# Performance work log

Measured on AMD Instinct MI355X. Metric: run time of the kernel, lower is better.

The kernel has to match this reference:

```python
import jax, jax.numpy as jnp
import numpy as np

N_NODES = 50000
N_EDGES = 100000
N_PAIRS = 1600000
IN_DIM = 2816
MAP_HID = 512
IN_CH = 512
HID_CH = 256
OUT_CH = 128


def _dense(x, W, b):
    return x @ W + b


def setup_inputs() -> dict:
    key = jax.random.key(0)
    ks = jax.random.split(key, 20)
    m_emb = jax.random.normal(ks[0], (N_NODES, IN_DIM), dtype=jnp.float32)
    he_v_idx_pos = jax.random.randint(ks[1], (N_PAIRS,), 0, N_NODES)
    he_e_idx_pos = jnp.sort(jax.random.randint(ks[2], (N_PAIRS,), 0, N_EDGES))
    he_v_idx_neg = jax.random.randint(ks[3], (N_PAIRS,), 0, N_NODES)
    he_e_idx_neg = jnp.sort(jax.random.randint(ks[4], (N_PAIRS,), 0, N_EDGES))

    def lin(k, din, dout):
        k1, k2 = jax.random.split(k)
        s = 1.0 / np.sqrt(din)
        W = jax.random.uniform(k1, (din, dout), minval=-s, maxval=s, dtype=jnp.float32)
        b = jax.random.uniform(k2, (dout,), minval=-s, maxval=s, dtype=jnp.float32)
        return W, b

    W0, b0 = lin(ks[5], IN_DIM, MAP_HID)
    W1, b1 = lin(ks[6], MAP_HID, MAP_HID)
    W2, b2 = lin(ks[7], MAP_HID, IN_CH)
    Wt1, bt1 = lin(ks[8], IN_CH, HID_CH)   # HGNN layer 1 theta
    Wt2, bt2 = lin(ks[9], HID_CH, OUT_CH)  # HGNN layer 2 theta

    return dict(
        m_emb=m_emb,
        he_v_idx_pos=he_v_idx_pos, he_e_idx_pos=he_e_idx_pos,
        he_v_idx_neg=he_v_idx_neg, he_e_idx_neg=he_e_idx_neg,
        W0=W0, b0=b0, W1=W1, b1=b1, W2=W2, b2=b2,
        Wt1=Wt1, bt1=bt1, Wt2=Wt2, bt2=bt2,
    )


def _hg_mean_aggr(X, v_idx, e_idx, n_edges, n_nodes):
    # v2e: mean of member-vertex features per hyperedge
    e_sum = jax.ops.segment_sum(X[v_idx], e_idx, num_segments=n_edges)
    e_cnt = jax.ops.segment_sum(jnp.ones((v_idx.shape[0],), X.dtype), e_idx, num_segments=n_edges)
    Y = e_sum / jnp.maximum(e_cnt, 1.0)[:, None]
    # e2v: mean of incident-hyperedge features per vertex
    v_sum = jax.ops.segment_sum(Y[e_idx], v_idx, num_segments=n_nodes)
    v_cnt = jax.ops.segment_sum(jnp.ones((e_idx.shape[0],), X.dtype), v_idx, num_segments=n_nodes)
    Xo = v_sum / jnp.maximum(v_cnt, 1.0)[:, None]
    return Xo, Y


def _hgnn_layer(X, v_idx, e_idx, W, b, is_last):
    X = _dense(X, W, b)
    Xo, Y = _hg_mean_aggr(X, v_idx, e_idx, N_EDGES, N_NODES)
    if not is_last:
        Xo = jax.nn.relu(Xo)  # dropout = identity in eval
    return Xo, Y


def reference(m_emb, he_v_idx_pos, he_e_idx_pos, he_v_idx_neg, he_e_idx_neg,
              W0, b0, W1, b1, W2, b2, Wt1, bt1, Wt2, bt2):
    h = jax.nn.relu(_dense(m_emb, W0, b0))
    h = jax.nn.relu(_dense(h, W1, b1))
    feat = _dense(h, W2, b2)  # [N, IN_CH]
    # num_dgnn = 0 -> skip directional conv loop
    X1, X2 = feat, feat
    X1, Y_pos = _hgnn_layer(X1, he_v_idx_pos, he_e_idx_pos, Wt1, bt1, False)
    X2, Y_neg = _hgnn_layer(X2, he_v_idx_neg, he_e_idx_neg, Wt1, bt1, False)
    X1, Y_pos = _hgnn_layer(X1, he_v_idx_pos, he_e_idx_pos, Wt2, bt2, True)
    X2, Y_neg = _hgnn_layer(X2, he_v_idx_neg, he_e_idx_neg, Wt2, bt2, True)
    return (X1, X2, Y_pos, Y_neg)
```

## Files before the change

kernel.cpp:

```cpp
#include <hip/hip_runtime.h>

#define NP 1600000
#define NNODES 50000
#define NEDGES 100000

typedef short bf16x8 __attribute__((ext_vector_type(8)));
typedef short short4b __attribute__((ext_vector_type(4)));
typedef float f32x4 __attribute__((ext_vector_type(4)));
typedef unsigned short ushort_t;

static __device__ __forceinline__ ushort_t f2bf_rne(float f) {
    __bf16 b = (__bf16)f;
    return __builtin_bit_cast(ushort_t, b);
}
static __device__ __forceinline__ float bf2f(ushort_t h) {
    union { float f; unsigned int u; } v; v.u = ((unsigned int)h) << 16;
    return v.f;
}
static __device__ __forceinline__ void addbf8(float* a, uint4 u) {
    unsigned int uu[4] = {u.x, u.y, u.z, u.w};
#pragma unroll
    for (int q = 0; q < 4; ++q) {
        union { float f; unsigned int v; } lo, hi;
        lo.v = uu[q] << 16; hi.v = uu[q] & 0xffff0000u;
        a[2 * q]     += lo.f;
        a[2 * q + 1] += hi.f;
    }
}

static __device__ __forceinline__ void gload_lds16(const void* g, void* lds) {
    __builtin_amdgcn_global_load_lds(
        (const __attribute__((address_space(1))) unsigned int*)g,
        (__attribute__((address_space(3))) unsigned int*)lds, 16, 0, 0);
}

template<bool AF32, bool DORELU, int EPI>
__global__ __launch_bounds__(256, 3) void gemm_bf1(
    const float* __restrict__ Af, const ushort_t* __restrict__ Ab,
    const ushort_t* __restrict__ Bth,
    const float* __restrict__ bias,
    float* __restrict__ Cf, ushort_t* __restrict__ Cb,
    int M, int N, int K)
{
    __shared__ ushort_t As [4][129][8];
    __shared__ ushort_t BsH[4][129][8];

    const int tid = threadIdx.x;
    const int wid = tid >> 6;
    const int lane = tid & 63;

    const int nwg = gridDim.x * gridDim.y;
    const int wg  = blockIdx.y * gridDim.x + blockIdx.x;
    const int q = nwg >> 3, r = nwg & 7;
    const int xcd = wg & 7, loc = wg >> 3;
    const int swz = (xcd < r) ? (xcd * (q + 1) + loc)
                              : (r * (q + 1) + (xcd - r) * q + loc);
    const int bn0 = (int)(swz % gridDim.x) * 128;
    const int bm0 = (int)(swz / gridDim.x) * 128;

    const int wrow0 = (wid >> 1) * 64;
    const int wcol0 = (wid & 1) * 64;
    const int kgl = lane >> 4;
    const int r16 = lane & 15;

    f32x4 acc[4][4];
#pragma unroll
    for (int i = 0; i < 4; ++i)
#pragma unroll
        for (int j = 0; j < 4; ++j) acc[i][j] = (f32x4)0.f;

    const int nk = K >> 5;

    const int a_kq   = tid & 7;
    const int a_row0 = tid >> 3;
    const float* aBase[4];
    float4 aPre[4];
    if constexpr (AF32) {
#pragma unroll
        for (int cch = 0; cch < 4; ++cch) {
            int row = cch * 32 + a_row0;
            int rr = bm0 + row; if (rr > M - 1) rr = M - 1;
            aBase[cch] = Af + (size_t)rr * K + a_kq * 4;
            aPre[cch] = *(const float4*)(aBase[cch]);
        }
    }

    for (int kt = 0; kt < nk; ++kt) {
        __syncthreads();
#pragma unroll
        for (int h = 0; h < 2; ++h) {
            int cc = bn0 + h * 64 + lane;
            gload_lds16(Bth + (size_t)cc * K + kt * 32 + wid * 8,
                        &BsH[wid][h * 64][0]);
        }
        if constexpr (AF32) {
#pragma unroll
            for (int cch = 0; cch < 4; ++cch) {
                int row = cch * 32 + a_row0;
                float4 v = aPre[cch];
                short4b hi;
                hi[0] = (short)f2bf_rne(v.x); hi[1] = (short)f2bf_rne(v.y);
                hi[2] = (short)f2bf_rne(v.z); hi[3] = (short)f2bf_rne(v.w);
                int kg = a_kq >> 1, j0 = (a_kq & 1) * 4;
                *(short4b*)&As[kg][row][j0] = hi;
            }
        } else {
#pragma unroll
            for (int h = 0; h < 2; ++h) {
                int rr = bm0 + h * 64 + lane; if (rr > M - 1) rr = M - 1;
                gload_lds16(Ab + (size_t)rr * K + kt * 32 + wid * 8,
                            &As[wid][h * 64][0]);
            }
        }
        __syncthreads();

        if constexpr (AF32) {
            if (kt + 1 < nk) {
#pragma unroll
                for (int cch = 0; cch < 4; ++cch)
                    aPre[cch] = *(const float4*)(aBase[cch] + (kt + 1) * 32);
            }
        }

        bf16x8 ah[4], bh[4];
#pragma unroll
        for (int mi = 0; mi < 4; ++mi)
            ah[mi] = *(const bf16x8*)&As[kgl][wrow0 + mi * 16 + r16][0];
#pragma unroll
        for (int ni = 0; ni < 4; ++ni)
            bh[ni] = *(const bf16x8*)&BsH[kgl][wcol0 + ni * 16 + r16][0];
#pragma unroll
        for (int mi = 0; mi < 4; ++mi)
#pragma unroll
            for (int ni = 0; ni < 4; ++ni)
                acc[mi][ni] = __builtin_amdgcn_mfma_f32_16x16x32_bf16(ah[mi], bh[ni], acc[mi][ni], 0, 0, 0);
    }

    const int rg4 = (lane >> 4) * 4;
#pragma unroll
    for (int ni = 0; ni < 4; ++ni) {
        int gcol = bn0 + wcol0 + ni * 16 + r16;
        float bb = bias[gcol];
#pragma unroll
        for (int mi = 0; mi < 4; ++mi)
#pragma unroll
            for (int rg = 0; rg < 4; ++rg) {
                int grow = bm0 + wrow0 + mi * 16 + rg4 + rg;
                if (grow < M) {
                    float v = acc[mi][ni][rg] + bb;
                    if constexpr (DORELU) v = fmaxf(v, 0.f);
                    if constexpr (EPI == 0) Cf[(size_t)grow * N + gcol] = v;
                    else                    Cb[(size_t)grow * N + gcol] = f2bf_rne(v);
                }
            }
    }
}

__global__ __launch_bounds__(256) void prep_csr(
    const float* __restrict__ W0, const float* __restrict__ W1,
    const float* __restrict__ W2, const float* __restrict__ Wt1,
    const float* __restrict__ Wt2,
    ushort_t* __restrict__ W0t, ushort_t* __restrict__ W1t,
    ushort_t* __restrict__ W2t, ushort_t* __restrict__ Wt1t,
    ushort_t* __restrict__ Wt2t,
    const int* __restrict__ ePos, const int* __restrict__ eNeg,
    const int* __restrict__ vPos, const int* __restrict__ vNeg,
    int* __restrict__ e_off, int* __restrict__ v_cnt)
{
    const int bsel = blockIdx.x;
    if (bsel >= 2080) {
        const int rel = bsel - 2080;
        const int sign = rel >> 10;
        const int* e_idx = sign ? eNeg : ePos;
        const int* v_idx = sign ? vNeg : vPos;
        int* o  = e_off + sign * (NEDGES + 1);
        int* vc = v_cnt + sign * NNODES;
        int i = (rel & 1023) * 256 + threadIdx.x;
        const int stride = 1024 * 256;
        for (; i < NP; i += stride) {
            int cur = e_idx[i];
            int prev = (i > 0) ? e_idx[i - 1] : -1;
            for (int e = prev + 1; e <= cur; ++e) o[e] = i;
            if (i == NP - 1)
                for (int e = cur + 1; e <= NEDGES; ++e) o[e] = NP;
            atomicAdd(&vc[v_idx[i]], 1);
        }
        return;
    }
    const float* W; ushort_t* H; int K, N, nx, rel;
    if (bsel < 1408)      { W = W0;  H = W0t;  K = 2816; N = 512; nx = 16; rel = bsel; }
    else if (bsel < 1664) { W = W1;  H = W1t;  K = 512;  N = 512; nx = 16; rel = bsel - 1408; }
    else if (bsel < 1920) { W = W2;  H = W2t;  K = 512;  N = 512; nx = 16; rel = bsel - 1664; }
    else if (bsel < 2048) { W = Wt1; H = Wt1t; K = 512;  N = 256; nx = 8;  rel = bsel - 1920; }
    else                  { W = Wt2; H = Wt2t; K = 256;  N = 128; nx = 4;  rel = bsel - 2048; }
    const int n0 = (rel % nx) * 32, k0 = (rel / nx) * 32;

    __shared__ float T[32][33];
    const int c = threadIdx.x & 31, r8 = threadIdx.x >> 5;
#pragma unroll
    for (int i = 0; i < 4; ++i)
        T[r8 + i * 8][c] = W[(size_t)(k0 + r8 + i * 8) * N + n0 + c];
    __syncthreads();
#pragma unroll
    for (int i = 0; i < 4; ++i) {
        int nr = r8 + i * 8;
        H[(size_t)(n0 + nr) * K + k0 + c] = f2bf_rne(T[c][nr]);
    }
}

__global__ __launch_bounds__(1024) void exscan2(const int* __restrict__ cnt,
                                                int* __restrict__ off)
{
    const int sign = blockIdx.x;
    const int* c = cnt + sign * NNODES;
    int* o = off + sign * (NNODES + 1);
    __shared__ int sums[1024];
    const int t = threadIdx.x;
    const int per = (NNODES + 1023) >> 10;
    const int b = t * per;
    const int e = min(b + per, NNODES);
    int s = 0;
    for (int i = b; i < e; ++i) s += c[i];
    sums[t] = s;
    __syncthreads();
    for (int d = 1; d < 1024; d <<= 1) {
        int v = (t >= d) ? sums[t - d] : 0;
        __syncthreads();
        sums[t] += v;
        __syncthreads();
    }
    int run = (t > 0) ? sums[t - 1] : 0;
    for (int i = b; i < e; ++i) { o[i] = run; run += c[i]; }
    if (t == 1023) o[NNODES] = run;
}

__global__ void scatter_both(const int* __restrict__ vPos, const int* __restrict__ vNeg,
                             const int* __restrict__ ePos, const int* __restrict__ eNeg,
                             const int* __restrict__ v_off, int* __restrict__ v_cnt,
                             int* __restrict__ e_by_v)
{
    const int sign = blockIdx.y;
    const int* v_idx = sign ? vNeg : vPos;
    const int* e_idx = sign ? eNeg : ePos;
    const int* vo = v_off + sign * (NNODES + 1);
    int* vc = v_cnt + sign * NNODES;
    int* ebv = e_by_v + sign * NP;
    int i = blockIdx.x * blockDim.x + threadIdx.x;
    int stride = gridDim.x * blockDim.x;
    for (; i < NP; i += stride) {
        int v = v_idx[i];
        int pos = atomicSub(&vc[v], 1) - 1;
        ebv[vo[v] + pos] = e_idx[i];
    }
}

template<bool SRCBF, int C, bool DORELU, int EPI>
__global__ __launch_bounds__(256) void seg_mean2(
    const void* __restrict__ src, long long src_stride,
    const int* __restrict__ idx0, const int* __restrict__ idx1,
    const int* __restrict__ off_base, int off_stride,
    float* __restrict__ dstf, long long dstf_stride,
    ushort_t* __restrict__ dB, long long dB_stride,
    int nseg)
{
    constexpr int ES  = SRCBF ? 2 : 4;
    constexpr int LPR = (C * ES) / 16;
    constexpr int MPI = 64 / LPR;
    constexpr int CPL = 16 / ES;

    const int sign = blockIdx.y;
    const int* idx = sign ? idx1 : idx0;
    const int* off = off_base + (size_t)sign * off_stride;

    const int wave = threadIdx.x >> 6, lane = threadIdx.x & 63;
    const int s = blockIdx.x * 4 + wave;
    if (s >= nseg) return;
    const int b = off[s], e = off[s + 1];
    const int sub = lane / LPR;
    const int cbase = (lane % LPR) * CPL;

    float a0[CPL], a1[CPL], a2[CPL], a3[CPL];
#pragma unroll
    for (int k = 0; k < CPL; ++k) { a0[k] = 0.f; a1[k] = 0.f; a2[k] = 0.f; a3[k] = 0.f; }

    int j = b + sub;
    if constexpr (SRCBF) {
        const ushort_t* sp = (const ushort_t*)src + (size_t)sign * src_stride;
        for (; j + 3 * MPI < e; j += 4 * MPI) {
            int i0 = idx[j], i1 = idx[j + MPI], i2 = idx[j + 2 * MPI], i3 = idx[j + 3 * MPI];
            uint4 u0 = *(const uint4*)(sp + (size_t)i0 * C + cbase);
            uint4 u1 = *(const uint4*)(sp + (size_t)i1 * C + cbase);
            uint4 u2 = *(const uint4*)(sp + (size_t)i2 * C + cbase);
            uint4 u3 = *(const uint4*)(sp + (size_t)i3 * C + cbase);
            addbf8(a0, u0); addbf8(a1, u1); addbf8(a2, u2); addbf8(a3, u3);
        }
        for (; j < e; j += MPI) {
            uint4 u = *(const uint4*)(sp + (size_t)idx[j] * C + cbase);
            addbf8(a0, u);
        }
    } else {
        const float* sp = (const float*)src + (size_t)sign * src_stride;
        for (; j + 3 * MPI < e; j += 4 * MPI) {
            int i0 = idx[j], i1 = idx[j + MPI], i2 = idx[j + 2 * MPI], i3 = idx[j + 3 * MPI];
            float4 v0 = *(const float4*)(sp + (size_t)i0 * C + cbase);
            float4 v1 = *(const float4*)(sp + (size_t)i1 * C + cbase);
            float4 v2 = *(const float4*)(sp + (size_t)i2 * C + cbase);
            float4 v3 = *(const float4*)(sp + (size_t)i3 * C + cbase);
            a0[0] += v0.x; a0[1] += v0.y; a0[2] += v0.z; a0[3] += v0.w;
            a1[0] += v1.x; a1[1] += v1.y; a1[2] += v1.z; a1[3] += v1.w;
            a2[0] += v2.x; a2[1] += v2.y; a2[2] += v2.z; a2[3] += v2.w;
            a3[0] += v3.x; a3[1] += v3.y; a3[2] += v3.z; a3[3] += v3.w;
        }
        for (; j < e; j += MPI) {
            float4 v = *(const float4*)(sp + (size_t)idx[j] * C + cbase);
            a0[0] += v.x; a0[1] += v.y; a0[2] += v.z; a0[3] += v.w;
        }
    }

    float acc[CPL];
#pragma unroll
    for (int k = 0; k < CPL; ++k) acc[k] = (a0[k] + a1[k]) + (a2[k] + a3[k]);

#pragma unroll
    for (int st = LPR; st < 64; st <<= 1)
#pragma unroll
        for (int k = 0; k < CPL; ++k)
            acc[k] += __shfl_xor(acc[k], st);

    if (lane < LPR) {
        const float inv = 1.f / fmaxf((float)(e - b), 1.f);
#pragma unroll
        for (int k = 0; k < CPL; ++k) {
            float v = acc[k] * inv;
            if constexpr (DORELU) v = fmaxf(v, 0.f);
            if constexpr (EPI == 0) {
                (dstf + (size_t)sign * dstf_stride)[(size_t)s * C + cbase + k] = v;
            } else if constexpr (EPI == 1) {
                (dB + (size_t)sign * dB_stride)[(size_t)s * C + cbase + k] = f2bf_rne(v);
            } else {
                (dstf + (size_t)sign * dstf_stride)[(size_t)s * C + cbase + k] = v;
                (dB + (size_t)sign * dB_stride)[(size_t)s * C + cbase + k] = f2bf_rne(v);
            }
        }
    }
}

extern "C" void kernel_launch(void* const* d_in, const int* in_sizes, int n_in,
                              void* d_out, int out_size, void* d_ws, size_t ws_size,
                              hipStream_t stream)
{
    const float* m_emb = (const float*)d_in[0];
    const int*   v_pos = (const int*)d_in[1];
    const int*   e_pos = (const int*)d_in[2];
    const int*   v_neg = (const int*)d_in[3];
    const int*   e_neg = (const int*)d_in[4];
    const float* W0  = (const float*)d_in[5];
    const float* b0  = (const float*)d_in[6];
    const float* W1  = (const float*)d_in[7];
    const float* b1  = (const float*)d_in[8];
    const float* W2  = (const float*)d_in[9];
    const float* b2  = (const float*)d_in[10];
    const float* Wt1 = (const float*)d_in[11];
    const float* bt1 = (const float*)d_in[12];
    const float* Wt2 = (const float*)d_in[13];
    const float* bt2 = (const float*)d_in[14];
    float* out = (float*)d_out;

    char* p = (char*)d_ws;
    auto carve = [&](size_t bytes) { char* r = p; p += (bytes + 255) & ~(size_t)255; return r; };
    const size_t NA = (size_t)NNODES * 512;
    ushort_t* regionA = (ushort_t*)carve(NA * 2);
    ushort_t* h1b  = (ushort_t*)carve(NA * 2);
    ushort_t* Y1b  = (ushort_t*)carve((size_t)2 * NEDGES * 256 * 2);
    ushort_t* Xt1b = (ushort_t*)carve((size_t)NNODES * 256 * 2);
    ushort_t* Xt2b = (ushort_t*)carve((size_t)2 * NNODES * 128 * 2);
    ushort_t* Y2b  = (ushort_t*)carve((size_t)2 * NEDGES * 128 * 2);

    ushort_t* h0b   = regionA;
    ushort_t* featb = regionA;
    ushort_t* X1b   = h1b;

    ushort_t* W0t  = (ushort_t*)carve((size_t)512 * 2816 * 2);
    ushort_t* W1t  = (ushort_t*)carve((size_t)512 * 512 * 2);
    ushort_t* W2t  = (ushort_t*)carve((size_t)512 * 512 * 2);
    ushort_t* Wt1t = (ushort_t*)carve((size_t)256 * 512 * 2);
    ushort_t* Wt2t = (ushort_t*)carve((size_t)128 * 256 * 2);
    int* e_off  = (int*)carve((size_t)2 * (NEDGES + 1) * 4);
    int* v_off  = (int*)carve((size_t)2 * (NNODES + 1) * 4);
    int* e_by_v = (int*)carve((size_t)2 * NP * 4);
    int* v_cnt  = (int*)carve((size_t)2 * NNODES * 4);

    const int MB = (NNODES + 127) / 128;
    const int MB2 = (2 * NNODES + 127) / 128;

    hipMemsetAsync(v_cnt, 0, (size_t)2 * NNODES * 4, stream);
    prep_csr<<<4128, 256, 0, stream>>>(
        W0, W1, W2, Wt1, Wt2,
        W0t, W1t, W2t, Wt1t, Wt2t,
        e_pos, e_neg, v_pos, v_neg, e_off, v_cnt);
    exscan2<<<2, 1024, 0, stream>>>(v_cnt, v_off);
    scatter_both<<<dim3(1024, 2), 256, 0, stream>>>(v_pos, v_neg, e_pos, e_neg,
                                                    v_off, v_cnt, e_by_v);

    gemm_bf1<true, true, 1><<<dim3(4, MB), 256, 0, stream>>>(
        m_emb, nullptr, W0t, b0, nullptr, h0b, NNODES, 512, 2816);
    gemm_bf1<false, true, 1><<<dim3(4, MB), 256, 0, stream>>>(
        nullptr, h0b, W1t, b1, nullptr, h1b, NNODES, 512, 512);
    gemm_bf1<false, false, 1><<<dim3(4, MB), 256, 0, stream>>>(
        nullptr, h1b, W2t, b2, nullptr, featb, NNODES, 512, 512);

    gemm_bf1<false, false, 1><<<dim3(2, MB), 256, 0, stream>>>(
        nullptr, featb, Wt1t, bt1, nullptr, Xt1b, NNODES, 256, 512);

    seg_mean2<true, 256, false, 1><<<dim3(NEDGES / 4, 2), 256, 0, stream>>>(
        Xt1b, 0, v_pos, v_neg, e_off, NEDGES + 1,
        nullptr, 0, Y1b, (long long)NEDGES * 256, NEDGES);
    seg_mean2<true, 256, true, 1><<<dim3(NNODES / 4, 2), 256, 0, stream>>>(
        Y1b, (long long)NEDGES * 256, e_by_v, e_by_v + NP, v_off, NNODES + 1,
        nullptr, 0, X1b, (long long)NNODES * 256, NNODES);

    gemm_bf1<false, false, 1><<<dim3(1, MB2), 256, 0, stream>>>(
        nullptr, X1b, Wt2t, bt2, nullptr, Xt2b, 2 * NNODES, 128, 256);

    seg_mean2<true, 128, false, 3><<<dim3(NEDGES / 4, 2), 256, 0, stream>>>(
        Xt2b, (long long)NNODES * 128, v_pos, v_neg, e_off, NEDGES + 1,
        out + 12800000, 12800000LL, Y2b, (long long)NEDGES * 128, NEDGES);
    seg_mean2<true, 128, false, 0><<<dim3(NNODES / 4, 2), 256, 0, stream>>>(
        Y2b, (long long)NEDGES * 128, e_by_v, e_by_v + NP, v_off, NNODES + 1,
        out, 6400000LL, nullptr, 0, NNODES);
}
```

Measured before the change: 1.702 ms.

## Split segment-mean gathers into column slices with multiple segments per wave

The segment-mean kernel is rewritten so that each block handles one 32-column slice of the feature rows for one sign. Each wave now processes four consecutive segments, and the block index interleaves slices and signs. Each gather load covers only a narrow column slice, so more segment members are loaded in parallel and concurrently running blocks work on the same slice. The intent is better cache locality for the random row gathers. In exchange, the per-segment index reads and the cross-lane reduction are repeated for every slice, and each wave has less unrolling.

```diff
diff --git a/kernel.cpp b/kernel.cpp
--- a/kernel.cpp
+++ b/kernel.cpp
@@ -254,92 +254,77 @@
     }
 }
 
-template<bool SRCBF, int C, bool DORELU, int EPI>
-__global__ __launch_bounds__(256) void seg_mean2(
-    const void* __restrict__ src, long long src_stride,
+template<int C, int NSLICE, int SPW, bool DORELU, int EPI>
+__global__ __launch_bounds__(256) void seg_mean3(
+    const ushort_t* __restrict__ src, long long src_stride,
     const int* __restrict__ idx0, const int* __restrict__ idx1,
     const int* __restrict__ off_base, int off_stride,
     float* __restrict__ dstf, long long dstf_stride,
     ushort_t* __restrict__ dB, long long dB_stride,
     int nseg)
 {
-    constexpr int ES  = SRCBF ? 2 : 4;
-    constexpr int LPR = (C * ES) / 16;
+    constexpr int CPS = C / NSLICE;
+    constexpr int LPR = CPS / 8;
     constexpr int MPI = 64 / LPR;
-    constexpr int CPL = 16 / ES;
-
-    const int sign = blockIdx.y;
+    constexpr int COMBO = 2 * NSLICE;
+
+    const int bid = blockIdx.x;
+    const int combo = bid & (COMBO - 1);
+    const int slice = combo & (NSLICE - 1);
+    const int sign  = combo / NSLICE;
+
+    const int wave = threadIdx.x >> 6, lane = threadIdx.x & 63;
+    const int s0 = ((bid / COMBO) * 4 + wave) * SPW;
+
     const int* idx = sign ? idx1 : idx0;
     const int* off = off_base + (size_t)sign * off_stride;
-
-    const int wave = threadIdx.x >> 6, lane = threadIdx.x & 63;
-    const int s = blockIdx.x * 4 + wave;
-    if (s >= nseg) return;
-    const int b = off[s], e = off[s + 1];
+    const ushort_t* sp = src + (size_t)sign * src_stride + slice * CPS;
     const int sub = lane / LPR;
-    const int cbase = (lane % LPR) * CPL;
-
-    float a0[CPL], a1[CPL], a2[CPL], a3[CPL];
-#pragma unroll
-    for (int k = 0; k < CPL; ++k) { a0[k] = 0.f; a1[k] = 0.f; a2[k] = 0.f; a3[k] = 0.f; }
-
-    int j = b + sub;
-    if constexpr (SRCBF) {
-        const ushort_t* sp = (const ushort_t*)src + (size_t)sign * src_stride;
-        for (; j + 3 * MPI < e; j += 4 * MPI) {
-            int i0 = idx[j], i1 = idx[j + MPI], i2 = idx[j + 2 * MPI], i3 = idx[j + 3 * MPI];
-            uint4 u0 = *(const uint4*)(sp + (size_t)i0 * C + cbase);
-            uint4 u1 = *(const uint4*)(sp + (size_t)i1 * C + cbase);
-            uint4 u2 = *(const uint4*)(sp + (size_t)i2 * C + cbase);
-            uint4 u3 = *(const uint4*)(sp + (size_t)i3 * C + cbase);
-            addbf8(a0, u0); addbf8(a1, u1); addbf8(a2, u2); addbf8(a3, u3);
+    const int cl  = (lane % LPR) * 8;
+
+    const int send = min(s0 + SPW, nseg);
+    for (int s = s0; s < send; ++s) {
+        const int b = off[s], e = off[s + 1];
+        float a0[8], a1[8];
+#pragma unroll
+        for (int k = 0; k < 8; ++k) { a0[k] = 0.f; a1[k] = 0.f; }
+
+        int j = b + sub;
+        for (; j + MPI < e; j += 2 * MPI) {
+            int i0 = idx[j], i1 = idx[j + MPI];
+            uint4 u0 = *(const uint4*)(sp + (size_t)i0 * C + cl);
+            uint4 u1 = *(const uint4*)(sp + (size_t)i1 * C + cl);
+            addbf8(a0, u0); addbf8(a1, u1);
         }
         for (; j < e; j += MPI) {
-            uint4 u = *(const uint4*)(sp + (size_t)idx[j] * C + cbase);
+            uint4 u = *(const uint4*)(sp + (size_t)idx[j] * C + cl);
             addbf8(a0, u);
         }
-    } else {
-        const float* sp = (const float*)src + (size_t)sign * src_stride;
-        for (; j + 3 * MPI < e; j += 4 * MPI) {
-            int i0 = idx[j], i1 = idx[j + MPI], i2 = idx[j + 2 * MPI], i3 = idx[j + 3 * MPI];
-            float4 v0 = *(const float4*)(sp + (size_t)i0 * C + cbase);
-            float4 v1 = *(const float4*)(sp + (size_t)i1 * C + cbase);
-            float4 v2 = *(const float4*)(sp + (size_t)i2 * C + cbase);
-            float4 v3 = *(const float4*)(sp + (size_t)i3 * C + cbase);
-            a0[0] += v0.x; a0[1] += v0.y; a0[2] += v0.z; a0[3] += v0.w;
-            a1[0] += v1.x; a1[1] += v1.y; a1[2] += v1.z; a1[3] += v1.w;
-            a2[0] += v2.x; a2[1] += v2.y; a2[2] += v2.z; a2[3] += v2.w;
-            a3[0] += v3.x; a3[1] += v3.y; a3[2] += v3.z; a3[3] += v3.w;
-        }
-        for (; j < e; j += MPI) {
-            float4 v = *(const float4*)(sp + (size_t)idx[j] * C + cbase);
-            a0[0] += v.x; a0[1] += v.y; a0[2] += v.z; a0[3] += v.w;
-        }
-    }
-
-    float acc[CPL];
-#pragma unroll
-    for (int k = 0; k < CPL; ++k) acc[k] = (a0[k] + a1[k]) + (a2[k] + a3[k]);
-
-#pragma unroll
-    for (int st = LPR; st < 64; st <<= 1)
-#pragma unroll
-        for (int k = 0; k < CPL; ++k)
-            acc[k] += __shfl_xor(acc[k], st);
-
-    if (lane < LPR) {
-        const float inv = 1.f / fmaxf((float)(e - b), 1.f);
-#pragma unroll
-        for (int k = 0; k < CPL; ++k) {
-            float v = acc[k] * inv;
-            if constexpr (DORELU) v = fmaxf(v, 0.f);
-            if constexpr (EPI == 0) {
-                (dstf + (size_t)sign * dstf_stride)[(size_t)s * C + cbase + k] = v;
-            } else if constexpr (EPI == 1) {
-                (dB + (size_t)sign * dB_stride)[(size_t)s * C + cbase + k] = f2bf_rne(v);
-            } else {
-                (dstf + (size_t)sign * dstf_stride)[(size_t)s * C + cbase + k] = v;
-                (dB + (size_t)sign * dB_stride)[(size_t)s * C + cbase + k] = f2bf_rne(v);
+
+        float acc[8];
+#pragma unroll
+        for (int k = 0; k < 8; ++k) acc[k] = a0[k] + a1[k];
+#pragma unroll
+        for (int st = LPR; st < 64; st <<= 1)
+#pragma unroll
+            for (int k = 0; k < 8; ++k)
+                acc[k] += __shfl_xor(acc[k], st);
+
+        if (lane < LPR) {
+            const float inv = 1.f / fmaxf((float)(e - b), 1.f);
+            const size_t obase = (size_t)s * C + slice * CPS + cl;
+#pragma unroll
+            for (int k = 0; k < 8; ++k) {
+                float v = acc[k] * inv;
+                if constexpr (DORELU) v = fmaxf(v, 0.f);
+                if constexpr (EPI == 0) {
+                    (dstf + (size_t)sign * dstf_stride)[obase + k] = v;
+                } else if constexpr (EPI == 1) {
+                    (dB + (size_t)sign * dB_stride)[obase + k] = f2bf_rne(v);
+                } else {
+                    (dstf + (size_t)sign * dstf_stride)[obase + k] = v;
+                    (dB + (size_t)sign * dB_stride)[obase + k] = f2bf_rne(v);
+                }
             }
         }
     }
@@ -412,20 +397,20 @@
     gemm_bf1<false, false, 1><<<dim3(2, MB), 256, 0, stream>>>(
         nullptr, featb, Wt1t, bt1, nullptr, Xt1b, NNODES, 256, 512);
 
-    seg_mean2<true, 256, false, 1><<<dim3(NEDGES / 4, 2), 256, 0, stream>>>(
+    seg_mean3<256, 8, 4, false, 1><<<16 * ((NEDGES + 15) / 16), 256, 0, stream>>>(
         Xt1b, 0, v_pos, v_neg, e_off, NEDGES + 1,
         nullptr, 0, Y1b, (long long)NEDGES * 256, NEDGES);
-    seg_mean2<true, 256, true, 1><<<dim3(NNODES / 4, 2), 256, 0, stream>>>(
+    seg_mean3<256, 8, 4, true, 1><<<16 * ((NNODES + 15) / 16), 256, 0, stream>>>(
         Y1b, (long long)NEDGES * 256, e_by_v, e_by_v + NP, v_off, NNODES + 1,
         nullptr, 0, X1b, (long long)NNODES * 256, NNODES);
 
     gemm_bf1<false, false, 1><<<dim3(1, MB2), 256, 0, stream>>>(
         nullptr, X1b, Wt2t, bt2, nullptr, Xt2b, 2 * NNODES, 128, 256);
 
-    seg_mean2<true, 128, false, 3><<<dim3(NEDGES / 4, 2), 256, 0, stream>>>(
+    seg_mean3<128, 4, 4, false, 3><<<8 * ((NEDGES + 15) / 16), 256, 0, stream>>>(
         Xt2b, (long long)NNODES * 128, v_pos, v_neg, e_off, NEDGES + 1,
         out + 12800000, 12800000LL, Y2b, (long long)NEDGES * 128, NEDGES);
-    seg_mean2<true, 128, false, 0><<<dim3(NNODES / 4, 2), 256, 0, stream>>>(
+    seg_mean3<128, 4, 4, false, 0><<<8 * ((NNODES + 15) / 16), 256, 0, stream>>>(
         Y2b, (long long)NEDGES * 128, e_by_v, e_by_v + NP, v_off, NNODES + 1,
         out, 6400000LL, nullptr, 0, NNODES);
 }
```

Result: slower. 2.415 ms (+41.9%).
